# Kernel tuning notes

Hardware: AMD Instinct MI355X
Metric: run time of the kernel (lower is better)

## Reference

```python
import jax, jax.numpy as jnp
import numpy as np

LN_EPS = 1e-5
BN_EPS = 1e-5
N_TARGETS = 7


def setup_inputs() -> dict:
    key = jax.random.key(0)
    ks = jax.random.split(key, 12)
    B, N, W, Fin = 64, 40, 256, 64
    H, D = 4, 32
    C = H * D  # gat_out = 128
    L, K = 4, 3  # tcn layers / kernel
    FC = 128
    x = jax.random.normal(ks[0], (B, N, W, Fin), dtype=jnp.float32)
    adj = (jax.random.uniform(ks[1], (N, N)) < 0.3).astype(jnp.float32)
    adj = jnp.maximum(adj, jnp.eye(N, dtype=jnp.float32))  # self-loops
    s = 0.05
    return {
        "x": x,
        "adj": adj,
        "gat_w": jax.random.normal(ks[2], (C, Fin), dtype=jnp.float32) * s,
        "a_src": jax.random.normal(ks[3], (H, D), dtype=jnp.float32) * s,
        "a_dst": jax.random.normal(ks[4], (H, D), dtype=jnp.float32) * s,
        "ln_g": jnp.ones((C,), jnp.float32),
        "ln_b": jnp.zeros((C,), jnp.float32),
        "c1w": jax.random.normal(ks[5], (L, C, C, K), dtype=jnp.float32) * s,
        "c1b": jnp.zeros((L, C), jnp.float32),
        "c2w": jax.random.normal(ks[6], (L, C, C, K), dtype=jnp.float32) * s,
        "c2b": jnp.zeros((L, C), jnp.float32),
        "bn1s": jnp.ones((L, C), jnp.float32),
        "bn1b": jnp.zeros((L, C), jnp.float32),
        "bn1m": jnp.zeros((L, C), jnp.float32),
        "bn1v": jnp.ones((L, C), jnp.float32),
        "bn2s": jnp.ones((L, C), jnp.float32),
        "bn2b": jnp.zeros((L, C), jnp.float32),
        "bn2m": jnp.zeros((L, C), jnp.float32),
        "bn2v": jnp.ones((L, C), jnp.float32),
        "f1w": jax.random.normal(ks[7], (FC, C), dtype=jnp.float32) * s,
        "f1b": jnp.zeros((FC,), jnp.float32),
        "f2w": jax.random.normal(ks[8], (1, FC), dtype=jnp.float32) * s,
        "f2b": jnp.zeros((1,), jnp.float32),
    }


def reference(x, adj, gat_w, a_src, a_dst, ln_g, ln_b,
              c1w, c1b, c2w, c2b,
              bn1s, bn1b, bn1m, bn1v, bn2s, bn2b, bn2m, bn2v,
              f1w, f1b, f2w, f2b):
    B, N, W, Fin = x.shape
    H, D = a_src.shape
    C = H * D
    # --- GAT, vectorized over all W timesteps at once (same math as the per-t loop) ---
    h = jnp.einsum('bnwf,of->bnwo', x, gat_w).reshape(B, N, W, H, D)
    e_src = jnp.einsum('bnwhd,hd->bnwh', h, a_src)  # (B,N,W,H)
    e_dst = jnp.einsum('bnwhd,hd->bnwh', h, a_dst)
    # scores[b,i,w,h,j] = leaky_relu(e_src[b,i] + e_dst[b,j])
    scores = e_src[:, :, :, :, None] + jnp.transpose(e_dst, (0, 2, 3, 1))[:, None]  # (B,N,W,H,N)
    scores = jax.nn.leaky_relu(scores, 0.2)
    mask = adj[None, :, None, None, :] != 0
    scores = jnp.where(mask, scores, -1e9)
    attn = jax.nn.softmax(scores, axis=-1)  # softmax over destination j
    gat = jnp.einsum('bnwhj,bjwhd->bnwhd', attn, h).reshape(B, N, W, C)
    # --- LayerNorm over feature dim ---
    mu = gat.mean(-1, keepdims=True)
    var = gat.var(-1, keepdims=True)
    g = (gat - mu) / jnp.sqrt(var + LN_EPS) * ln_g + ln_b
    # --- TCN over per-node temporal sequences: (B*N, C, W) ---
    seq = jnp.transpose(g.reshape(B * N, W, C), (0, 2, 1))
    K = c1w.shape[-1]

    def bn(z, s, b, m, v):
        return (z - m[None, :, None]) / jnp.sqrt(v[None, :, None] + BN_EPS) * s[None, :, None] + b[None, :, None]

    def cconv(z, w, b, dil):
        pad = (K - 1) * dil  # causal left-padding
        y = jax.lax.conv_general_dilated(z, w, window_strides=(1,), padding=[(pad, 0)],
                                         rhs_dilation=(dil,), dimension_numbers=('NCH', 'OIH', 'NCH'))
        return y + b[None, :, None]

    cur = seq
    for i in range(c1w.shape[0]):  # fixed small number of TCN blocks
        dil = 2 ** i
        o = jax.nn.gelu(bn(cconv(cur, c1w[i], c1b[i], dil), bn1s[i], bn1b[i], bn1m[i], bn1v[i]), approximate=False)
        o = jax.nn.gelu(bn(cconv(o, c2w[i], c2b[i], dil), bn2s[i], bn2b[i], bn2m[i], bn2v[i]), approximate=False)
        cur = jax.nn.gelu(o + cur, approximate=False)  # residual is Identity (in_ch == out_ch)
    h_last = cur[:, :, -1].reshape(B, N, C)
    t = h_last[:, :N_TARGETS, :]  # target_indices = range(7)
    z = jax.nn.gelu(jnp.einsum('bnc,hc->bnh', t, f1w) + f1b, approximate=False)
    logits = (jnp.einsum('bnh,oh->bno', z, f2w) + f2b)[..., 0]  # (B, 7)
    return logits
```

## Files before the change

kernel.cpp:

```cpp
#include <hip/hip_runtime.h>
#include <hip/hip_bf16.h>
#include <math.h>

#define Bb   64
#define Nn   40
#define Ww   256
#define FIN  64
#define Hh   4
#define Dd   32
#define Cc   128
#define NT   7
#define FC   128
#define WT   61
#define W0   195
#define PSTRIDE 520
#define HS   132

#define SEQHI_OFF  0u
#define SEQ_BYTES  (448u * WT * Cc * 2u)
#define SEQLO_OFF  (SEQHI_OFF + SEQ_BYTES)
#define WBH_OFF    (SEQLO_OFF + SEQ_BYTES)
#define WB_BYTES   (8u * 4u * 24u * 64u * 8u * 2u)
#define WBL_OFF    (WBH_OFF + WB_BYTES)
#define PSB_OFF    (WBL_OFF + WB_BYTES)
#define PSS_OFF    (PSB_OFF + 4096u)
#define PSH_OFF    (PSS_OFF + 4096u)
#define WGH_OFF    (PSH_OFF + 4096u)
#define WGL_OFF    (WGH_OFF + 16384u)
#define WPHASE_US  49152u

typedef __attribute__((ext_vector_type(8)))  short short8;
typedef __attribute__((ext_vector_type(16))) float f32x16;

__device__ __forceinline__ float gelu_exact(float v) {
    return 0.5f * v * (1.0f + erff(v * 0.70710678118654752440f));
}
__device__ __forceinline__ float b2f(ushort u) {
    union { uint i; float f; } c; c.i = ((uint)u) << 16; return c.f;
}
__device__ __forceinline__ void split_bf16(float v, ushort& h, ushort& l) {
    __hip_bfloat16 bh = __float2bfloat16(v);
    float fh = __bfloat162float(bh);
    __hip_bfloat16 bl = __float2bfloat16(v - fh);
    h = *(ushort*)&bh; l = *(ushort*)&bl;
}

__global__ __launch_bounds__(256) void prep_kernel(
    const float* __restrict__ c1w, const float* __restrict__ c1b,
    const float* __restrict__ c2w, const float* __restrict__ c2b,
    const float* __restrict__ bn1s, const float* __restrict__ bn1b,
    const float* __restrict__ bn1m, const float* __restrict__ bn1v,
    const float* __restrict__ bn2s, const float* __restrict__ bn2b,
    const float* __restrict__ bn2m, const float* __restrict__ bn2v,
    const float* __restrict__ gat_w,
    char* __restrict__ ws)
{
    if (blockIdx.x < 192) {
        const int t = blockIdx.x * 256 + threadIdx.x;
        const int lane  = t & 63;
        const int kstep = (t >> 6) % 24;
        const int nt    = ((t >> 6) / 24) & 3;
        const int p     = (t >> 6) / 96;
        const int l = p >> 1, cv = p & 1;
        const int co = nt * 32 + (lane & 31);
        const float* wsrc = cv ? c2w : c1w;
        ushort* wbh = (ushort*)(ws + WBH_OFF);
        ushort* wbl = (ushort*)(ws + WBL_OFF);
#pragma unroll
        for (int j = 0; j < 8; ++j) {
            const int k  = kstep * 16 + ((lane >> 5) << 3) + j;
            const int kk = k >> 7, ci = k & 127;
            const float w = wsrc[((size_t)(l * Cc + co) * Cc + ci) * 3 + kk];
            ushort h, lo; split_bf16(w, h, lo);
            wbh[(size_t)t * 8 + j] = h;
            wbl[(size_t)t * 8 + j] = lo;
        }
    } else if (blockIdx.x == 192) {
        float* psb = (float*)(ws + PSB_OFF);
        float* pss = (float*)(ws + PSS_OFF);
        float* psh = (float*)(ws + PSH_OFF);
        for (int idx = threadIdx.x; idx < 1024; idx += 256) {
            const int p = idx >> 7, co = idx & 127;
            const int l = p >> 1, cv = p & 1;
            const int lc = l * Cc + co;
            const float s  = cv ? bn2s[lc] : bn1s[lc];
            const float bb = cv ? bn2b[lc] : bn1b[lc];
            const float m  = cv ? bn2m[lc] : bn1m[lc];
            const float vv = cv ? bn2v[lc] : bn1v[lc];
            const float cb = cv ? c2b[lc] : c1b[lc];
            const float scale = s * rsqrtf(vv + 1e-5f);
            pss[idx] = scale;
            psh[idx] = bb - m * scale;
            psb[idx] = cb;
        }
    } else {
        ushort* wgh = (ushort*)(ws + WGH_OFF);
        ushort* wgl = (ushort*)(ws + WGL_OFF);
#pragma unroll
        for (int it = 0; it < 4; ++it) {
            const int t = it * 256 + threadIdx.x;
            const int lane = t & 63;
            const int ks   = (t >> 6) & 3;
            const int nt   = t >> 8;
            const int co   = nt * 32 + (lane & 31);
#pragma unroll
            for (int j = 0; j < 8; ++j) {
                const int k = ks * 16 + ((lane >> 5) << 3) + j;
                ushort h, lo; split_bf16(gat_w[co * FIN + k], h, lo);
                wgh[t * 8 + j] = h;
                wgl[t * 8 + j] = lo;
            }
        }
    }
}

__global__ __launch_bounds__(256) void gat_ln_kernel(
    const float* __restrict__ x, const float* __restrict__ adj,
    const char* __restrict__ ws_ro,
    const float* __restrict__ a_src, const float* __restrict__ a_dst,
    const float* __restrict__ ln_g, const float* __restrict__ ln_b,
    ushort* __restrict__ seq_hi, ushort* __restrict__ seq_lo)
{
    __shared__ __align__(16) ushort xa_hi[8 * PSTRIDE];
    __shared__ __align__(16) ushort xa_lo[8 * PSTRIDE];
    __shared__ __align__(16) float h_lds[Nn * HS];
    __shared__ __align__(16) float e_lds[2 * Nn * Hh];
    __shared__ __align__(16) float attn_lds[NT * Hh * Nn];
    __shared__ __align__(16) float g_lds[NT * Cc];

    const int tid = threadIdx.x;
    const int blk = blockIdx.x;
    const int b   = blk / WT;
    const int tau = blk % WT;
    const int w   = W0 + tau;

    for (int idx = tid; idx < Nn * 8; idx += 256) {
        const int n  = idx >> 3;
        const int oc = idx & 7;
        const float* src = x + ((size_t)(b * Nn + n) * Ww + w) * FIN + oc * 8;
        const float4 f0 = *(const float4*)(src);
        const float4 f1 = *(const float4*)(src + 4);
        ushort h[8], l[8];
        split_bf16(f0.x, h[0], l[0]); split_bf16(f0.y, h[1], l[1]);
        split_bf16(f0.z, h[2], l[2]); split_bf16(f0.w, h[3], l[3]);
        split_bf16(f1.x, h[4], l[4]); split_bf16(f1.y, h[5], l[5]);
        split_bf16(f1.z, h[6], l[6]); split_bf16(f1.w, h[7], l[7]);
        const int dst = oc * PSTRIDE + n * 8;
        *(uint4*)(xa_hi + dst) = *(uint4*)h;
        *(uint4*)(xa_lo + dst) = *(uint4*)l;
    }
    for (int idx = tid; idx < 8 * (64 - Nn); idx += 256) {
        const int oc = idx / (64 - Nn);
        const int n  = Nn + idx % (64 - Nn);
        const int dst = oc * PSTRIDE + n * 8;
        uint4 z; z.x = z.y = z.z = z.w = 0u;
        *(uint4*)(xa_hi + dst) = z;
        *(uint4*)(xa_lo + dst) = z;
    }
    __syncthreads();

    {
        const int wave = tid >> 6;
        const int lane = tid & 63;
        const int nt   = wave;
        const int q2   = lane >> 5;
        const int m32  = lane & 31;
        const ushort* WGH = (const ushort*)(ws_ro + WGH_OFF);
        const ushort* WGL = (const ushort*)(ws_ro + WGL_OFF);

        f32x16 acc0, acc1;
#pragma unroll
        for (int i = 0; i < 16; ++i) { acc0[i] = 0.f; acc1[i] = 0.f; }

#pragma unroll
        for (int ks = 0; ks < 4; ++ks) {
            const size_t wo = ((size_t)((nt * 4 + ks) * 64 + lane)) * 8;
            const short8 bh = *(const short8*)(WGH + wo);
            const short8 bl = *(const short8*)(WGL + wo);
            const int pan = (ks * 2 + q2) * PSTRIDE;
            const short8 ah0 = *(const short8*)(xa_hi + pan + m32 * 8);
            const short8 al0 = *(const short8*)(xa_lo + pan + m32 * 8);
            const short8 ah1 = *(const short8*)(xa_hi + pan + (32 + m32) * 8);
            const short8 al1 = *(const short8*)(xa_lo + pan + (32 + m32) * 8);
            acc0 = __builtin_amdgcn_mfma_f32_32x32x16_bf16(ah0, bh, acc0, 0, 0, 0);
            acc0 = __builtin_amdgcn_mfma_f32_32x32x16_bf16(al0, bh, acc0, 0, 0, 0);
            acc0 = __builtin_amdgcn_mfma_f32_32x32x16_bf16(ah0, bl, acc0, 0, 0, 0);
            acc1 = __builtin_amdgcn_mfma_f32_32x32x16_bf16(ah1, bh, acc1, 0, 0, 0);
            acc1 = __builtin_amdgcn_mfma_f32_32x32x16_bf16(al1, bh, acc1, 0, 0, 0);
            acc1 = __builtin_amdgcn_mfma_f32_32x32x16_bf16(ah1, bl, acc1, 0, 0, 0);
        }

        const int co = nt * 32 + m32;
#pragma unroll
        for (int reg = 0; reg < 16; ++reg) {
            const int n = (reg & 3) + 8 * (reg >> 2) + 4 * q2;
            h_lds[n * HS + co] = acc0[reg];
        }
#pragma unroll
        for (int reg = 0; reg < 4; ++reg) {
            const int n = 32 + reg + 4 * q2;
            if (n < Nn) h_lds[n * HS + co] = acc1[reg];
        }
    }
    __syncthreads();

    for (int u = tid; u < 2 * Nn * Hh; u += 256) {
        const int s  = u & 1;
        const int hh = (u >> 1) & 3;
        const int n  = u >> 3;
        const float* av = (s ? a_dst : a_src) + hh * Dd;
        const float* hp = h_lds + n * HS + hh * Dd;
        float acc = 0.f;
#pragma unroll
        for (int i = 0; i < 8; ++i) {
            const float4 hv = *(const float4*)(hp + i * 4);
            const float4 avv = *(const float4*)(av + i * 4);
            acc += hv.x * avv.x + hv.y * avv.y + hv.z * avv.z + hv.w * avv.w;
        }
        e_lds[s * (Nn * Hh) + n * Hh + hh] = acc;
    }
    __syncthreads();

    if (tid < NT * Hh) {
        const int n  = tid >> 2;
        const int hh = tid & 3;
        const float es = e_lds[n * Hh + hh];
        float sc[Nn];
        float mx = -1e30f;
#pragma unroll
        for (int j = 0; j < Nn; ++j) {
            float s = es + e_lds[Nn * Hh + j * Hh + hh];
            s = (s > 0.f) ? s : 0.2f * s;
            if (adj[n * Nn + j] == 0.0f) s = -1e9f;
            sc[j] = s;
            mx = fmaxf(mx, s);
        }
        float sum = 0.f;
#pragma unroll
        for (int j = 0; j < Nn; ++j) { const float p = expf(sc[j] - mx); sc[j] = p; sum += p; }
        const float inv = 1.0f / sum;
#pragma unroll
        for (int j = 0; j < Nn; ++j)
            attn_lds[(n * Hh + hh) * Nn + j] = sc[j] * inv;
    }
    __syncthreads();

    if (tid < NT * 32) {
        const int n    = tid >> 5;
        const int cq   = tid & 31;
        const int c0   = cq * 4;
        const int head = cq >> 3;
        const float* ap = attn_lds + (n * Hh + head) * Nn;
        float4 acc = make_float4(0.f, 0.f, 0.f, 0.f);
        for (int j = 0; j < Nn; ++j) {
            const float a = ap[j];
            const float4 hv = *(const float4*)(h_lds + j * HS + c0);
            acc.x += a * hv.x; acc.y += a * hv.y;
            acc.z += a * hv.z; acc.w += a * hv.w;
        }
        *(float4*)(g_lds + n * Cc + c0) = acc;
    }
    __syncthreads();

    if (tid < NT * 32) {
        const int n = tid >> 5, lane = tid & 31;
        const float4 v = ((const float4*)(g_lds + n * Cc))[lane];
        float s  = v.x + v.y + v.z + v.w;
        float sq = v.x*v.x + v.y*v.y + v.z*v.z + v.w*v.w;
#pragma unroll
        for (int off = 16; off; off >>= 1) {
            s  += __shfl_xor(s, off, 32);
            sq += __shfl_xor(sq, off, 32);
        }
        const float mu   = s * (1.0f / Cc);
        const float rstd = rsqrtf(sq * (1.0f / Cc) - mu * mu + 1e-5f);
        const float4 gg = ((const float4*)ln_g)[lane];
        const float4 bb = ((const float4*)ln_b)[lane];
        float o0 = (v.x - mu) * rstd * gg.x + bb.x;
        float o1 = (v.y - mu) * rstd * gg.y + bb.y;
        float o2 = (v.z - mu) * rstd * gg.z + bb.z;
        float o3 = (v.w - mu) * rstd * gg.w + bb.w;
        const int r = b * NT + n;
        ushort4 uh, ul;
        split_bf16(o0, uh.x, ul.x);
        split_bf16(o1, uh.y, ul.y);
        split_bf16(o2, uh.z, ul.z);
        split_bf16(o3, uh.w, ul.w);
        const int p  = (lane >> 2) * 2 + ((lane >> 1) & 1);
        const int j0 = (lane & 1) * 4;
        const size_t off = ((size_t)(r * 16 + p) * WT + tau) * 8 + j0;
        *(ushort4*)(seq_hi + off) = uh;
        *(ushort4*)(seq_lo + off) = ul;
    }
}

__device__ __forceinline__ void conv_mfma(
    const ushort* in_hi, const ushort* in_lo,
    ushort* out_hi, ushort* out_lo,
    const ushort* __restrict__ wbh, const ushort* __restrict__ wbl,
    const float* __restrict__ psb, const float* __restrict__ pss,
    const float* __restrict__ psh,
    const int tau0, const int d, const int mt, const int nt,
    const int lane, const bool residual)
{
    const int m  = lane & 31;
    const int q2 = lane >> 5;
    const int co = nt * 32 + m;

    f32x16 acc;
#pragma unroll
    for (int i = 0; i < 16; ++i) acc[i] = 0.f;

    const int mbase = mt * 32 + m;
    for (int ks = 0; ks < 24; ++ks) {
        const int kk = ks >> 3;
        int rowA = mbase - (2 - kk) * d;
        rowA = rowA < 0 ? 0 : rowA;
        const int aoff = (((ks & 7) << 1) + q2) * PSTRIDE + rowA * 8;
        const short8 ah = *(const short8*)(in_hi + aoff);
        const short8 al = *(const short8*)(in_lo + aoff);
        const size_t wo = ((size_t)(nt * 24 + ks) * 64 + lane) * 8;
        const short8 bh = *(const short8*)(wbh + wo);
        const short8 bl = *(const short8*)(wbl + wo);
        acc = __builtin_amdgcn_mfma_f32_32x32x16_bf16(ah, bh, acc, 0, 0, 0);
        acc = __builtin_amdgcn_mfma_f32_32x32x16_bf16(al, bh, acc, 0, 0, 0);
        acc = __builtin_amdgcn_mfma_f32_32x32x16_bf16(ah, bl, acc, 0, 0, 0);
    }

    const float bsv = psb[co], scv = pss[co], shv = psh[co];
    const int colb = ((co >> 4) * 2 + ((co >> 3) & 1)) * PSTRIDE + (co & 7);
#pragma unroll
    for (int reg = 0; reg < 16; ++reg) {
        const int row = (reg & 3) + 8 * (reg >> 2) + 4 * q2;
        const int tau = mt * 32 + row;
        if (tau >= tau0 && tau <= 60) {
            float v = (acc[reg] + bsv) * scv + shv;
            v = gelu_exact(v);
            const int off = colb + tau * 8;
            if (residual) {
                const float rc = b2f(out_hi[off]) + b2f(out_lo[off]);
                v = gelu_exact(v + rc);
            }
            ushort uh, ul; split_bf16(v, uh, ul);
            out_hi[off] = uh; out_lo[off] = ul;
        }
    }
}

__global__ __launch_bounds__(512) void tcn_head_kernel(
    const char* __restrict__ ws,
    const float* __restrict__ f1w, const float* __restrict__ f1b,
    const float* __restrict__ f2w, const float* __restrict__ f2b,
    float* __restrict__ out)
{
    __shared__ __align__(16) ushort cur_hi[16 * PSTRIDE];
    __shared__ __align__(16) ushort cur_lo[16 * PSTRIDE];
    __shared__ __align__(16) ushort o1_hi [16 * PSTRIDE];
    __shared__ __align__(16) ushort o1_lo [16 * PSTRIDE];
    __shared__ float red[FC];

    const int tid = threadIdx.x;
    const int r   = blockIdx.x;

    const ushort* seq_hi = (const ushort*)(ws + SEQHI_OFF);
    const ushort* seq_lo = (const ushort*)(ws + SEQLO_OFF);
    const ushort* WBH    = (const ushort*)(ws + WBH_OFF);
    const ushort* WBL    = (const ushort*)(ws + WBL_OFF);
    const float*  PSB    = (const float*)(ws + PSB_OFF);
    const float*  PSS    = (const float*)(ws + PSS_OFF);
    const float*  PSH    = (const float*)(ws + PSH_OFF);

    {
        const size_t base = (size_t)r * (16 * WT * 8);
        for (int i = tid; i < 16 * WT; i += 512) {
            const int p = i / WT, row = i - p * WT;
            const int dst = p * PSTRIDE + row * 8;
            *(uint4*)(cur_hi + dst) = *(const uint4*)(seq_hi + base + i * 8);
            *(uint4*)(cur_lo + dst) = *(const uint4*)(seq_lo + base + i * 8);
        }
    }
    __syncthreads();

    const int wave = tid >> 6;
    const int lane = tid & 63;
    const int nt   = wave & 3;
    const int mt   = wave >> 2;

    const int tau0_1[4] = {2, 8, 20, 44};
    const int tau0_2[4] = {4, 12, 28, 60};

#pragma unroll
    for (int l = 0; l < 4; ++l) {
        const int d  = 1 << l;
        const int p1 = 2 * l, p2 = 2 * l + 1;
        conv_mfma(cur_hi, cur_lo, o1_hi, o1_lo,
                  WBH + (size_t)p1 * WPHASE_US, WBL + (size_t)p1 * WPHASE_US,
                  PSB + p1 * Cc, PSS + p1 * Cc, PSH + p1 * Cc,
                  tau0_1[l], d, mt, nt, lane, false);
        __syncthreads();
        conv_mfma(o1_hi, o1_lo, cur_hi, cur_lo,
                  WBH + (size_t)p2 * WPHASE_US, WBL + (size_t)p2 * WPHASE_US,
                  PSB + p2 * Cc, PSS + p2 * Cc, PSH + p2 * Cc,
                  tau0_2[l], d, mt, nt, lane, true);
        __syncthreads();
    }

    if (tid < FC) {
        const float4* wr = (const float4*)(f1w + tid * Cc);
        float acc = 0.f;
#pragma unroll
        for (int i = 0; i < Cc / 4; ++i) {
            const float4 wv = wr[i];
            const int ci0 = i * 4;
            const int off = ((ci0 >> 4) * 2 + ((ci0 >> 3) & 1)) * PSTRIDE
                          + 60 * 8 + (ci0 & 7);
            acc += wv.x * (b2f(cur_hi[off + 0]) + b2f(cur_lo[off + 0]))
                 + wv.y * (b2f(cur_hi[off + 1]) + b2f(cur_lo[off + 1]))
                 + wv.z * (b2f(cur_hi[off + 2]) + b2f(cur_lo[off + 2]))
                 + wv.w * (b2f(cur_hi[off + 3]) + b2f(cur_lo[off + 3]));
        }
        red[tid] = gelu_exact(acc + f1b[tid]) * f2w[tid];
    }
    __syncthreads();
    if (tid < 64) {
        float v = red[tid] + red[tid + 64];
#pragma unroll
        for (int off = 32; off; off >>= 1) v += __shfl_xor(v, off, 64);
        if (tid == 0) out[r] = v + f2b[0];
    }
}

extern "C" void kernel_launch(void* const* d_in, const int* in_sizes, int n_in,
                              void* d_out, int out_size, void* d_ws, size_t ws_size,
                              hipStream_t stream) {
    const float* x     = (const float*)d_in[0];
    const float* adj   = (const float*)d_in[1];
    const float* gat_w = (const float*)d_in[2];
    const float* a_src = (const float*)d_in[3];
    const float* a_dst = (const float*)d_in[4];
    const float* ln_g  = (const float*)d_in[5];
    const float* ln_b  = (const float*)d_in[6];
    const float* c1w   = (const float*)d_in[7];
    const float* c1b   = (const float*)d_in[8];
    const float* c2w   = (const float*)d_in[9];
    const float* c2b   = (const float*)d_in[10];
    const float* bn1s  = (const float*)d_in[11];
    const float* bn1b  = (const float*)d_in[12];
    const float* bn1m  = (const float*)d_in[13];
    const float* bn1v  = (const float*)d_in[14];
    const float* bn2s  = (const float*)d_in[15];
    const float* bn2b  = (const float*)d_in[16];
    const float* bn2m  = (const float*)d_in[17];
    const float* bn2v  = (const float*)d_in[18];
    const float* f1w   = (const float*)d_in[19];
    const float* f1b   = (const float*)d_in[20];
    const float* f2w   = (const float*)d_in[21];
    const float* f2b   = (const float*)d_in[22];

    char* ws = (char*)d_ws;

    prep_kernel<<<194, 256, 0, stream>>>(c1w, c1b, c2w, c2b,
        bn1s, bn1b, bn1m, bn1v, bn2s, bn2b, bn2m, bn2v, gat_w, ws);

    gat_ln_kernel<<<Bb * WT, 256, 0, stream>>>(
        x, adj, ws, a_src, a_dst, ln_g, ln_b,
        (ushort*)(ws + SEQHI_OFF), (ushort*)(ws + SEQLO_OFF));

    tcn_head_kernel<<<Bb * NT, 512, 0, stream>>>(
        ws, f1w, f1b, f2w, f2b, (float*)d_out);
}
```

Before: 428.4 us.

## Prefetch conv weights in registers, split MFMA accumulators, batch residual loads

```diff
diff --git a/kernel.cpp b/kernel.cpp
--- a/kernel.cpp
+++ b/kernel.cpp
@@ -306,48 +306,81 @@
     const int m  = lane & 31;
     const int q2 = lane >> 5;
     const int co = nt * 32 + m;
-
-    f32x16 acc;
-#pragma unroll
-    for (int i = 0; i < 16; ++i) acc[i] = 0.f;
-
     const int mbase = mt * 32 + m;
+
+    const float bsv = psb[co], scv = pss[co], shv = psh[co];
+    const int colb = ((co >> 4) * 2 + ((co >> 3) & 1)) * PSTRIDE + (co & 7);
+
+    int rA0 = mbase - 2 * d; rA0 = rA0 < 0 ? 0 : rA0;
+    int rA1 = mbase - d;     rA1 = rA1 < 0 ? 0 : rA1;
+    const int rA2 = mbase;
+
+    const ushort* wb_h = wbh + (size_t)(nt * 24) * 512 + lane * 8;
+    const ushort* wb_l = wbl + (size_t)(nt * 24) * 512 + lane * 8;
+
+    f32x16 acc0, acc1;
+#pragma unroll
+    for (int i = 0; i < 16; ++i) { acc0[i] = 0.f; acc1[i] = 0.f; }
+
+    short8 WH[4], WL[4];
+#pragma unroll
+    for (int i = 0; i < 4; ++i) {
+        WH[i] = *(const short8*)(wb_h + i * 512);
+        WL[i] = *(const short8*)(wb_l + i * 512);
+    }
+
+#pragma unroll
     for (int ks = 0; ks < 24; ++ks) {
-        const int kk = ks >> 3;
-        int rowA = mbase - (2 - kk) * d;
-        rowA = rowA < 0 ? 0 : rowA;
+        const int slot = ks & 3;
+        const short8 bh = WH[slot];
+        const short8 bl = WL[slot];
+        if (ks + 4 < 24) {
+            WH[slot] = *(const short8*)(wb_h + (ks + 4) * 512);
+            WL[slot] = *(const short8*)(wb_l + (ks + 4) * 512);
+        }
+        const int kk   = ks >> 3;
+        const int rowA = (kk == 0) ? rA0 : (kk == 1 ? rA1 : rA2);
         const int aoff = (((ks & 7) << 1) + q2) * PSTRIDE + rowA * 8;
         const short8 ah = *(const short8*)(in_hi + aoff);
         const short8 al = *(const short8*)(in_lo + aoff);
-        const size_t wo = ((size_t)(nt * 24 + ks) * 64 + lane) * 8;
-        const short8 bh = *(const short8*)(wbh + wo);
-        const short8 bl = *(const short8*)(wbl + wo);
-        acc = __builtin_amdgcn_mfma_f32_32x32x16_bf16(ah, bh, acc, 0, 0, 0);
-        acc = __builtin_amdgcn_mfma_f32_32x32x16_bf16(al, bh, acc, 0, 0, 0);
-        acc = __builtin_amdgcn_mfma_f32_32x32x16_bf16(ah, bl, acc, 0, 0, 0);
-    }
-
-    const float bsv = psb[co], scv = pss[co], shv = psh[co];
-    const int colb = ((co >> 4) * 2 + ((co >> 3) & 1)) * PSTRIDE + (co & 7);
+        acc0 = __builtin_amdgcn_mfma_f32_32x32x16_bf16(ah, bh, acc0, 0, 0, 0);
+        acc1 = __builtin_amdgcn_mfma_f32_32x32x16_bf16(al, bh, acc1, 0, 0, 0);
+        if (ks & 1)
+            acc0 = __builtin_amdgcn_mfma_f32_32x32x16_bf16(ah, bl, acc0, 0, 0, 0);
+        else
+            acc1 = __builtin_amdgcn_mfma_f32_32x32x16_bf16(ah, bl, acc1, 0, 0, 0);
+    }
+#pragma unroll
+    for (int i = 0; i < 16; ++i) acc0[i] += acc1[i];
+
+    float rc[16];
+    if (residual) {
+#pragma unroll
+        for (int reg = 0; reg < 16; ++reg) {
+            const int row = (reg & 3) + 8 * (reg >> 2) + 4 * q2;
+            const int tau = mt * 32 + row;
+            const int off = colb + tau * 8;
+            rc[reg] = (tau >= tau0 && tau <= 60)
+                    ? (b2f(out_hi[off]) + b2f(out_lo[off])) : 0.f;
+        }
+    }
+
 #pragma unroll
     for (int reg = 0; reg < 16; ++reg) {
         const int row = (reg & 3) + 8 * (reg >> 2) + 4 * q2;
         const int tau = mt * 32 + row;
         if (tau >= tau0 && tau <= 60) {
-            float v = (acc[reg] + bsv) * scv + shv;
+            float v = (acc0[reg] + bsv) * scv + shv;
             v = gelu_exact(v);
+            if (residual) v = gelu_exact(v + rc[reg]);
+            ushort uh, ul; split_bf16(v, uh, ul);
             const int off = colb + tau * 8;
-            if (residual) {
-                const float rc = b2f(out_hi[off]) + b2f(out_lo[off]);
-                v = gelu_exact(v + rc);
-            }
-            ushort uh, ul; split_bf16(v, uh, ul);
             out_hi[off] = uh; out_lo[off] = ul;
         }
     }
 }
 
-__global__ __launch_bounds__(512) void tcn_head_kernel(
+__global__ __launch_bounds__(512, 4) void tcn_head_kernel(
     const char* __restrict__ ws,
     const float* __restrict__ f1w, const float* __restrict__ f1b,
     const float* __restrict__ f2w, const float* __restrict__ f2b,
```

Result: faster. 387.3 us (-9.6%).
